# Kernel tuning notes

Hardware: AMD Instinct MI355X
Metric: run time of the kernel (lower is better)

Reference implementation:

```python
import jax, jax.numpy as jnp
import numpy as np

B, N, OBS, H, A = 1024, 64, 128, 256, 16
NH = 4
HD = H // NH


def _linear_params(key, fan_in, fan_out):
    k1, k2 = jax.random.split(key)
    bound = 1.0 / np.sqrt(fan_in)
    W = jax.random.uniform(k1, (fan_out, fan_in), jnp.float32, -bound, bound)
    b = jax.random.uniform(k2, (fan_out,), jnp.float32, -bound, bound)
    return W, b


def setup_inputs() -> dict:
    key = jax.random.key(0)
    ks = jax.random.split(key, 10)
    obs = jax.random.normal(ks[0], (B, N, OBS), jnp.float32)
    adj = jax.random.randint(ks[1], (B, N, N), 0, 2).astype(jnp.float32)
    # guarantee every row has at least one neighbor (self-loop) so softmax is finite
    adj = jnp.maximum(adj, jnp.eye(N, dtype=jnp.float32)[None])
    W1, b1 = _linear_params(ks[2], OBS, H)
    W2, b2 = _linear_params(ks[3], H, H)
    Wq, bq = _linear_params(ks[4], H, H)
    Wk, bk = _linear_params(ks[5], H, H)
    Wv, bv = _linear_params(ks[6], H, H)
    Wo, bo = _linear_params(ks[7], H, H)
    Wc, bc = _linear_params(ks[8], H, H)
    W3, b3 = _linear_params(ks[9], H, A)
    return dict(obs=obs, adj=adj, W1=W1, b1=b1, W2=W2, b2=b2,
                Wq=Wq, bq=bq, Wk=Wk, bk=bk, Wv=Wv, bv=bv,
                Wo=Wo, bo=bo, Wc=Wc, bc=bc, W3=W3, b3=b3)


def reference(obs, adj, W1, b1, W2, b2, Wq, bq, Wk, bk, Wv, bv, Wo, bo, Wc, bc, W3, b3):
    lin = lambda x, W, b: jnp.einsum('bnd,od->bno', x, W) + b
    x = jax.nn.relu(lin(obs, W1, b1))
    x = jax.nn.relu(lin(x, W2, b2))
    # multi-head attention with adjacency mask
    def heads(t):  # [B,N,H] -> [B,NH,N,HD]
        return t.reshape(B, N, NH, HD).transpose(0, 2, 1, 3)
    q = heads(lin(x, Wq, bq))
    k = heads(lin(x, Wk, bk))
    v = heads(lin(x, Wv, bv))
    scores = jnp.einsum('bhqd,bhkd->bhqk', q, k) / np.sqrt(HD).astype(np.float32)
    scores = jnp.where(adj[:, None] == 0, -jnp.inf, scores)
    attn = jax.nn.softmax(scores, axis=-1)
    out = jnp.einsum('bhqk,bhkd->bhqd', attn, v)
    out = out.transpose(0, 2, 1, 3).reshape(B, N, H)
    x = lin(out, Wo, bo)
    # communication: adj @ fc(x)
    x = jnp.einsum('bnm,bmh->bnh', adj, lin(x, Wc, bc))
    return lin(x, W3, b3)
```

## Files before the change

kernel.cpp:

```cpp
#include <hip/hip_runtime.h>
#include <stdint.h>

typedef unsigned short u16;
typedef unsigned long long u64;
typedef __attribute__((ext_vector_type(8))) short short8;
typedef __attribute__((ext_vector_type(4))) float f32x4;

#define MFMA16 __builtin_amdgcn_mfma_f32_16x16x32_bf16

#define MTOT 65536

__device__ __forceinline__ u16 f2bf(float f) {
  union { float f; uint32_t u; } v; v.f = f;
  uint32_t r = v.u + 0x7FFFu + ((v.u >> 16) & 1u);
  return (u16)(r >> 16);
}

union U8 { short8 v; u16 u[8]; };
union U4 { u64 v; u16 u[4]; };

__device__ __forceinline__ void cp16(const void* g, void* l) {
  __builtin_amdgcn_global_load_lds(
      (const __attribute__((address_space(1))) void*)g,
      (__attribute__((address_space(3))) void*)l, 16, 0, 0);
}

__device__ __forceinline__ int swz(int row) { return ((row >> 1) & 3) << 4; }

__global__ __launch_bounds__(256) void k_l1(
    const float* __restrict__ Wc, const float* __restrict__ Wo,
    const float* __restrict__ bo, const float* __restrict__ bc,
    float* __restrict__ M1, float* __restrict__ bv,
    const float* __restrict__ W1, const float* __restrict__ W2,
    const float* __restrict__ Wq, const float* __restrict__ Wk,
    u16* o1, u16* o2, u16* oq, u16* ok,
    const float* __restrict__ adj, u64* __restrict__ adjm_g) {
  const int bid = blockIdx.x, tid = threadIdx.x;
  if (bid < 256) {
    __shared__ float wcr[256];
    __shared__ float red[4];
    const int j = bid, d = tid;
    wcr[d] = Wc[j * 256 + d];
    __syncthreads();
    float acc = 0.f;
    for (int i = 0; i < 256; i++) acc += wcr[i] * Wo[i * 256 + d];
    M1[j * 256 + d] = acc;
    float p = wcr[d] * bo[d];
    for (int off = 32; off >= 1; off >>= 1) p += __shfl_xor(p, off);
    if ((d & 63) == 0) red[d >> 6] = p;
    __syncthreads();
    if (d == 0) bv[j] = bc[j] + red[0] + red[1] + red[2] + red[3];
  } else if (bid < 368) {
    int off8 = (bid - 256) * 256 + tid;
    const float* src; u16* dst;
    if      (off8 <  4096) { src = W1; dst = o1; }
    else if (off8 < 12288) { src = W2; dst = o2; off8 -= 4096; }
    else if (off8 < 20480) { src = Wq; dst = oq; off8 -= 12288; }
    else                   { src = Wk; dst = ok; off8 -= 20480; }
    const int e = off8 * 8;
    f32x4 a = *(const f32x4*)(src + e);
    f32x4 b = *(const f32x4*)(src + e + 4);
    U8 pk;
#pragma unroll
    for (int j = 0; j < 4; j++) { pk.u[j] = f2bf(a[j]); pk.u[4 + j] = f2bf(b[j]); }
    *(short8*)(dst + e) = pk.v;
  } else {
    __shared__ u16 chunk[64][4];
    const int b = bid - 368;
    const int q = tid >> 2, qa = tid & 3;
    const float* ar = adj + ((size_t)b * 64 + q) * 64 + qa * 16;
    f32x4 a0 = *(const f32x4*)(ar);
    f32x4 a1 = *(const f32x4*)(ar + 4);
    f32x4 a2 = *(const f32x4*)(ar + 8);
    f32x4 a3 = *(const f32x4*)(ar + 12);
    unsigned m16 = 0;
#pragma unroll
    for (int i = 0; i < 4; i++) {
      m16 |= (unsigned)(a0[i] != 0.f) << i;
      m16 |= (unsigned)(a1[i] != 0.f) << (4 + i);
      m16 |= (unsigned)(a2[i] != 0.f) << (8 + i);
      m16 |= (unsigned)(a3[i] != 0.f) << (12 + i);
    }
    chunk[q][qa] = (u16)m16;
    __syncthreads();
    if (tid < 64)
      adjm_g[(size_t)b * 64 + tid] =
          (u64)chunk[tid][0] | ((u64)chunk[tid][1] << 16) |
          ((u64)chunk[tid][2] << 32) | ((u64)chunk[tid][3] << 48);
  }
}

template<int K, bool AF32>
__device__ __forceinline__ void gemm_full2(
    const void* __restrict__ Ain, const u16* __restrict__ W,
    const float* __restrict__ bias, u16* __restrict__ C,
    const int m0, const bool relu, char* smem) {
  const int tid = threadIdx.x;
  const int lane = tid & 63, wid = tid >> 6;
  const int wr = wid >> 1, wc = wid & 1;
  const int ro = lane & 15, hi = lane >> 4;

  f32x4 acc0[4][4], acc1[4][4];
#pragma unroll
  for (int m = 0; m < 4; m++)
#pragma unroll
    for (int n = 0; n < 4; n++) {
      acc0[m][n] = (f32x4){0.f, 0.f, 0.f, 0.f};
      acc1[m][n] = (f32x4){0.f, 0.f, 0.f, 0.f};
    }

  auto stage = [&](int buf, int k0) {
    char* Ax = smem + buf * 24576;
    char* Bx = Ax + 8192;
    if (AF32) {
      const float* Af = (const float*)Ain;
#pragma unroll
      for (int it = 0; it < 2; it++) {
        const int e = (tid + it * 256) * 8;
        const int r = e >> 5, c = e & 31;
        const float* s = Af + (size_t)(m0 + r) * K + k0 + c;
        f32x4 a = *(const f32x4*)s, b = *(const f32x4*)(s + 4);
        U8 pk;
#pragma unroll
        for (int j = 0; j < 4; j++) { pk.u[j] = f2bf(a[j]); pk.u[4 + j] = f2bf(b[j]); }
        *(short8*)(Ax + ((r * 64 + c * 2) ^ swz(r))) = pk.v;
      }
    } else {
      const u16* Ab = (const u16*)Ain;
#pragma unroll
      for (int i = 0; i < 2; i++) {
        const int boff = i * 4096 + wid * 1024;
        const int t = boff + lane * 16;
        const int row = t >> 6;
        const int cb = (t & 63) ^ swz(row);
        cp16(Ab + (size_t)(m0 + row) * K + k0 + (cb >> 1), Ax + boff);
      }
    }
#pragma unroll
    for (int i = 0; i < 4; i++) {
      const int boff = i * 4096 + wid * 1024;
      const int t = boff + lane * 16;
      const int row = t >> 6;
      const int cb = (t & 63) ^ swz(row);
      cp16(W + (size_t)row * K + k0 + (cb >> 1), Bx + boff);
    }
  };

  auto compute = [&](int buf) {
    char* Ax = smem + buf * 24576;
    char* Bx = Ax + 8192;
    short8 af[4], fb0[4], fb1[4];
#pragma unroll
    for (int m = 0; m < 4; m++) {
      const int row = wr * 64 + m * 16 + ro;
      af[m] = *(const short8*)(Ax + ((row * 64 + hi * 16) ^ swz(row)));
    }
#pragma unroll
    for (int n = 0; n < 4; n++) {
      const int r0 = wc * 64 + n * 16 + ro;
      fb0[n] = *(const short8*)(Bx + ((r0 * 64 + hi * 16) ^ swz(r0)));
      const int r1 = 128 + r0;
      fb1[n] = *(const short8*)(Bx + ((r1 * 64 + hi * 16) ^ swz(r1)));
    }
    __builtin_amdgcn_s_setprio(1);
#pragma unroll
    for (int m = 0; m < 4; m++)
#pragma unroll
      for (int n = 0; n < 4; n++) {
        acc0[m][n] = MFMA16(af[m], fb0[n], acc0[m][n], 0, 0, 0);
        acc1[m][n] = MFMA16(af[m], fb1[n], acc1[m][n], 0, 0, 0);
      }
    __builtin_amdgcn_s_setprio(0);
  };

  constexpr int NT = K / 32;
  if (AF32) {
    stage(0, 0);
    __syncthreads();
    int cur = 0;
    for (int k0 = 32; k0 < K; k0 += 32) {
      stage(cur ^ 1, k0);
      compute(cur);
      __syncthreads();
      cur ^= 1;
    }
    compute(cur);
    __syncthreads();
  } else {
    stage(0, 0);
    stage(1, 32);
#pragma unroll
    for (int t = 0; t < NT; ++t) {
      if (t == NT - 1) asm volatile("s_waitcnt vmcnt(0)" ::: "memory");
      else             asm volatile("s_waitcnt vmcnt(6)" ::: "memory");
      asm volatile("s_barrier" ::: "memory");
      compute(t & 1);
      asm volatile("s_barrier" ::: "memory");
      if (t + 2 < NT) stage(t & 1, (t + 2) * 32);
    }
  }

  u16 (*Cs)[136] = (u16(*)[136])smem;
  auto ep = [&](f32x4 (&acc)[4][4], const int n0) {
#pragma unroll
    for (int half = 0; half < 2; half++) {
      if (wr == half) {
#pragma unroll
        for (int n = 0; n < 4; n++) {
          const int col = wc * 64 + n * 16 + ro;
          const float bb = bias[n0 + col];
#pragma unroll
          for (int m = 0; m < 4; m++)
#pragma unroll
            for (int j = 0; j < 4; j++) {
              float val = acc[m][n][j] + bb;
              if (relu) val = fmaxf(val, 0.f);
              Cs[m * 16 + hi * 4 + j][col] = f2bf(val);
            }
        }
      }
      __syncthreads();
      for (int i = tid; i < 64 * 16; i += 256) {
        const int r = i >> 4, c = (i & 15) << 3;
        *(short8*)(C + (size_t)(m0 + half * 64 + r) * 256 + n0 + c) = *(short8*)&Cs[r][c];
      }
      __syncthreads();
    }
  };
  ep(acc0, 0);
  ep(acc1, 128);
}

__global__ __launch_bounds__(256, 2) void k_gemm1_prep2(
    const float* __restrict__ obs, const u16* __restrict__ W1b,
    const float* __restrict__ b1, u16* __restrict__ x1,
    const float* __restrict__ W3, const float* __restrict__ M1,
    const float* __restrict__ bvchain, const float* __restrict__ bvw,
    float* __restrict__ Wzf, float* __restrict__ bz) {
  __shared__ char smem[49152];
  if (blockIdx.x < 512) {
    gemm_full2<128, true>(obs, W1b, b1, x1, (int)blockIdx.x * 128, true, smem);
    return;
  }
  float* w3r = (float*)smem;
  float* red = (float*)(smem + 1024);
  const int a = blockIdx.x - 512, d = threadIdx.x;
  w3r[d] = W3[a * 256 + d];
  __syncthreads();
  float acc = 0.f;
  for (int j = 0; j < 256; j++) acc += w3r[j] * M1[j * 256 + d];
  Wzf[a * 256 + d] = acc;
  float p = w3r[d] * bvchain[d] + acc * bvw[d];
  for (int off = 32; off >= 1; off >>= 1) p += __shfl_xor(p, off);
  if ((d & 63) == 0) red[d >> 6] = p;
  __syncthreads();
  if (d == 0) bz[a] = red[0] + red[1] + red[2] + red[3];
}

__global__ __launch_bounds__(256, 2) void k_x2_prep3(
    const u16* __restrict__ x1, const u16* __restrict__ W2b,
    const float* __restrict__ b2, u16* __restrict__ x2,
    const float* __restrict__ Wzf, const float* __restrict__ Wv,
    u16* __restrict__ G) {
  __shared__ char smem[49152];
  if (blockIdx.x < 512) {
    gemm_full2<256, false>(x1, W2b, b2, x2, (int)blockIdx.x * 128, true, smem);
    return;
  }
  const int g = blockIdx.x - 512, d2 = threadIdx.x;
  const int h = g >> 4, a = g & 15;
  float* wzr = (float*)smem;
  if (d2 < 64) wzr[d2] = Wzf[a * 256 + h * 64 + d2];
  __syncthreads();
  float acc = 0.f;
#pragma unroll 8
  for (int d = 0; d < 64; d++) acc += wzr[d] * Wv[(size_t)(h * 64 + d) * 256 + d2];
  G[g * 256 + d2] = f2bf(acc);
}

__global__ __launch_bounds__(256, 2) void k_qk_gemmv(
    const u16* __restrict__ x2,
    const u16* __restrict__ Wqb, const float* __restrict__ bq, u16* __restrict__ Qg,
    const u16* __restrict__ Wkb, const float* __restrict__ bk, u16* __restrict__ Kg,
    const u16* __restrict__ G, u16* __restrict__ Vzt) {
  __shared__ char smem[49152];
  const int bid = blockIdx.x;
  if (bid < 1024) {
    const int q = bid >> 4, r = bid & 15;
    const int mt = q * 8 + (r & 7);
    const int sub = r >> 3;
    gemm_full2<256, false>(x2, sub ? Wkb : Wqb, sub ? bk : bq, sub ? Kg : Qg,
                           mt * 128, false, smem);
    return;
  }
  const int tid = threadIdx.x;
  const int lane = tid & 63, w = tid >> 6;
  const int ro = lane & 15, hi = lane >> 4;
  const int m0 = (bid - 1024) * 128;

  f32x4 acc[2][4];
#pragma unroll
  for (int m = 0; m < 2; m++)
#pragma unroll
    for (int n = 0; n < 4; n++) acc[m][n] = (f32x4){0.f, 0.f, 0.f, 0.f};

  auto stage = [&](int buf, int k0) {
    char* Ax = smem + buf * 12288;
    char* Bx = Ax + 8192;
#pragma unroll
    for (int i = 0; i < 2; i++) {
      const int boff = i * 4096 + w * 1024;
      const int t = boff + lane * 16;
      const int row = t >> 6;
      const int cb = (t & 63) ^ swz(row);
      cp16(x2 + (size_t)(m0 + row) * 256 + k0 + (cb >> 1), Ax + boff);
    }
    {
      const int boff = w * 1024;
      const int t = boff + lane * 16;
      const int row = t >> 6;
      const int cb = (t & 63) ^ swz(row);
      cp16(G + (size_t)row * 256 + k0 + (cb >> 1), Bx + boff);
    }
  };
  auto compute = [&](int buf) {
    char* Ax = smem + buf * 12288;
    char* Bx = Ax + 8192;
    short8 af[2], fb[4];
#pragma unroll
    for (int m = 0; m < 2; m++) {
      const int row = w * 32 + m * 16 + ro;
      af[m] = *(const short8*)(Ax + ((row * 64 + hi * 16) ^ swz(row)));
    }
#pragma unroll
    for (int n = 0; n < 4; n++) {
      const int row = n * 16 + ro;
      fb[n] = *(const short8*)(Bx + ((row * 64 + hi * 16) ^ swz(row)));
    }
    __builtin_amdgcn_s_setprio(1);
#pragma unroll
    for (int m = 0; m < 2; m++)
#pragma unroll
      for (int n = 0; n < 4; n++)
        acc[m][n] = MFMA16(af[m], fb[n], acc[m][n], 0, 0, 0);
    __builtin_amdgcn_s_setprio(0);
  };

  stage(0, 0);
  stage(1, 32);
#pragma unroll
  for (int t = 0; t < 8; ++t) {
    if (t == 7) asm volatile("s_waitcnt vmcnt(0)" ::: "memory");
    else        asm volatile("s_waitcnt vmcnt(3)" ::: "memory");
    asm volatile("s_barrier" ::: "memory");
    compute(t & 1);
    asm volatile("s_barrier" ::: "memory");
    if (t + 2 < 8) stage(t & 1, (t + 2) * 32);
  }

#pragma unroll
  for (int m = 0; m < 2; m++) {
    const int rbase = w * 32 + m * 16;
    const int bidx = (m0 >> 6) + (rbase >> 6);
    const int ke = (rbase + hi * 4) & 63;
#pragma unroll
    for (int n = 0; n < 4; n++) {
      const int c = n * 16 + ro;
      U4 pk;
#pragma unroll
      for (int j = 0; j < 4; j++) pk.u[j] = f2bf(acc[m][n][j]);
      *(u64*)(Vzt + (size_t)bidx * 4096 + (size_t)c * 64 + ke) = pk.v;
    }
  }
}

__global__ __launch_bounds__(256, 2) void attn_fused(
    const u16* __restrict__ Qg, const u16* __restrict__ Kg,
    const u16* __restrict__ Vzt, const u64* __restrict__ adjm_g,
    const float* __restrict__ bz, const float* __restrict__ b3,
    float* __restrict__ out) {
  __shared__ char sm_raw[36864];
  __shared__ u64 adjm[64];
  u16 (*Ps)[64][72] = (u16(*)[64][72])sm_raw;
  float (*Zs)[64][16] = (float(*)[64][16])sm_raw;

  const int b = blockIdx.x, tid = threadIdx.x;
  const int lane = tid & 63, w = tid >> 6;
  const int ro = lane & 15, hi = lane >> 4;
  const int hc = w * 64;
  const size_t base = (size_t)b * 64 * 256;

  if (tid < 64) adjm[tid] = adjm_g[(size_t)b * 64 + tid];

  short8 kb[4][2];
#pragma unroll
  for (int n = 0; n < 4; n++)
#pragma unroll
    for (int ks = 0; ks < 2; ks++)
      kb[n][ks] = *(const short8*)(Kg + base + (size_t)(n * 16 + ro) * 256 + hc + ks * 32 + hi * 8);

  f32x4 s[4][4];
#pragma unroll
  for (int m = 0; m < 4; m++) {
    short8 af[2];
#pragma unroll
    for (int ks = 0; ks < 2; ks++)
      af[ks] = *(const short8*)(Qg + base + (size_t)(m * 16 + ro) * 256 + hc + ks * 32 + hi * 8);
#pragma unroll
    for (int n = 0; n < 4; n++) s[m][n] = (f32x4){0.f, 0.f, 0.f, 0.f};
#pragma unroll
    for (int ks = 0; ks < 2; ks++)
#pragma unroll
      for (int n = 0; n < 4; n++)
        s[m][n] = MFMA16(af[ks], kb[n][ks], s[m][n], 0, 0, 0);
  }

  short8 vz[2];
#pragma unroll
  for (int ks = 0; ks < 2; ks++)
    vz[ks] = *(const short8*)(Vzt + (size_t)b * 4096 + (size_t)(hc / 4 + ro) * 64 + ks * 32 + hi * 8);

  __syncthreads();

#pragma unroll
  for (int m = 0; m < 4; m++) {
#pragma unroll
    for (int j = 0; j < 4; j++) {
      const int q = m * 16 + hi * 4 + j;
      const u64 msk = adjm[q];
      float sv[4], ev[4];
      float mx = -3.0e38f;
#pragma unroll
      for (int n = 0; n < 4; n++) {
        const bool on = (msk >> (n * 16 + ro)) & 1ull;
        sv[n] = on ? s[m][n][j] * 0.125f : -3.0e38f;
        mx = fmaxf(mx, sv[n]);
      }
      mx = fmaxf(mx, __shfl_xor(mx, 1));
      mx = fmaxf(mx, __shfl_xor(mx, 2));
      mx = fmaxf(mx, __shfl_xor(mx, 4));
      mx = fmaxf(mx, __shfl_xor(mx, 8));
      float sum = 0.f;
#pragma unroll
      for (int n = 0; n < 4; n++) {
        ev[n] = (sv[n] > -1.0e37f) ? __expf(sv[n] - mx) : 0.f;
        sum += ev[n];
      }
      sum += __shfl_xor(sum, 1);
      sum += __shfl_xor(sum, 2);
      sum += __shfl_xor(sum, 4);
      sum += __shfl_xor(sum, 8);
      const float inv = 1.0f / sum;
#pragma unroll
      for (int n = 0; n < 4; n++)
        Ps[w][q][n * 16 + ro] = f2bf(ev[n] * inv);
    }
  }

  f32x4 oz[4];
#pragma unroll
  for (int m = 0; m < 4; m++) {
    short8 pa[2];
    pa[0] = *(const short8*)&Ps[w][m * 16 + ro][hi * 8];
    pa[1] = *(const short8*)&Ps[w][m * 16 + ro][32 + hi * 8];
    oz[m] = (f32x4){0.f, 0.f, 0.f, 0.f};
#pragma unroll
    for (int ks = 0; ks < 2; ks++)
      oz[m] = MFMA16(pa[ks], vz[ks], oz[m], 0, 0, 0);
  }
  __syncthreads();

#pragma unroll
  for (int m = 0; m < 4; m++)
#pragma unroll
    for (int j = 0; j < 4; j++)
      Zs[w][m * 16 + hi * 4 + j][ro] = oz[m][j];
  __syncthreads();

  for (int i = tid; i < 1024; i += 256) {
    const int r = i >> 4, a = i & 15;
    Zs[0][r][a] += Zs[1][r][a] + Zs[2][r][a] + Zs[3][r][a];
  }
  __syncthreads();

  {
    const int n = tid >> 2, a4 = (tid & 3) << 2;
    const u64 msk = adjm[n];
    const float deg = (float)__popcll(msk);
    float a0 = 0.f, a1 = 0.f, a2 = 0.f, a3 = 0.f;
#pragma unroll 8
    for (int m = 0; m < 64; m++) {
      const float wv = (float)((msk >> m) & 1ull);
      f32x4 z = *(const f32x4*)&Zs[0][m][a4];
      a0 += wv * z[0]; a1 += wv * z[1]; a2 += wv * z[2]; a3 += wv * z[3];
    }
    f32x4 r;
    r[0] = a0 + b3[a4 + 0] + deg * bz[a4 + 0];
    r[1] = a1 + b3[a4 + 1] + deg * bz[a4 + 1];
    r[2] = a2 + b3[a4 + 2] + deg * bz[a4 + 2];
    r[3] = a3 + b3[a4 + 3] + deg * bz[a4 + 3];
    *(f32x4*)(out + ((size_t)b * 64 + n) * 16 + a4) = r;
  }
}

extern "C" void kernel_launch(void* const* d_in, const int* in_sizes, int n_in,
                              void* d_out, int out_size, void* d_ws, size_t ws_size,
                              hipStream_t stream) {
  const float* obs = (const float*)d_in[0];
  const float* adj = (const float*)d_in[1];
  const float* W1  = (const float*)d_in[2];
  const float* b1  = (const float*)d_in[3];
  const float* W2  = (const float*)d_in[4];
  const float* b2  = (const float*)d_in[5];
  const float* Wq  = (const float*)d_in[6];
  const float* bq  = (const float*)d_in[7];
  const float* Wk  = (const float*)d_in[8];
  const float* bk  = (const float*)d_in[9];
  const float* Wv  = (const float*)d_in[10];
  const float* bvw = (const float*)d_in[11];
  const float* Wo  = (const float*)d_in[12];
  const float* bo  = (const float*)d_in[13];
  const float* Wc  = (const float*)d_in[14];
  const float* bc  = (const float*)d_in[15];
  const float* W3  = (const float*)d_in[16];
  const float* b3  = (const float*)d_in[17];
  float* out = (float*)d_out;

  char* ws = (char*)d_ws;
  const size_t BIG = (size_t)MTOT * 256 * 2;
  u16* buf0 = (u16*)(ws);
  u16* buf1 = (u16*)(ws + BIG);
  u16* buf2 = (u16*)(ws + 2 * BIG);
  u16* buf3 = (u16*)(ws + 3 * BIG);
  char* p = ws + 4 * BIG;
  u16* W1b = (u16*)p;              p += 128 * 256 * 2;
  u16* W2b = (u16*)p;              p += 256 * 256 * 2;
  u16* Wqb = (u16*)p;              p += 256 * 256 * 2;
  u16* Wkb = (u16*)p;              p += 256 * 256 * 2;
  float* M1 = (float*)p;           p += 256 * 256 * 4;
  float* Wzf = (float*)p;          p += 16 * 256 * 4;
  u16* G   = (u16*)p;              p += 64 * 256 * 2;
  float* bv = (float*)p;           p += 256 * 4;
  float* bz = (float*)p;           p += 16 * 4;
  u64* adjm_g = (u64*)p;           p += (size_t)MTOT * 8;

  dim3 blk(256);
  k_l1<<<dim3(1392), blk, 0, stream>>>(Wc, Wo, bo, bc, M1, bv,
                                       W1, W2, Wq, Wk, W1b, W2b, Wqb, Wkb,
                                       adj, adjm_g);
  k_gemm1_prep2<<<dim3(528), blk, 0, stream>>>(obs, W1b, b1, buf0,
                                               W3, M1, bv, bvw, Wzf, bz);
  k_x2_prep3<<<dim3(576), blk, 0, stream>>>(buf0, W2b, b2, buf1, Wzf, Wv, G);
  k_qk_gemmv<<<dim3(1536), blk, 0, stream>>>(buf1, Wqb, bq, buf2,
                                             Wkb, bk, buf3, G, buf0);
  attn_fused<<<dim3(1024), blk, 0, stream>>>(buf2, buf3, buf0, adjm_g, bz, b3, out);
}
```

Before: 118.9 us.

## Fuse Vz projection into x2 GEMM epilogue and fold G prep into layer1 kernel

The x2 GEMM epilogue now stages bf16 output tiles in LDS and immediately multiplies them by the G matrix with MFMA to produce Vzt. This removes the separate GEMV blocks that re-read x2 from global memory in the QK kernel. The G computation moves into the prep blocks of the first GEMM kernel, which drops the intermediate Wzf buffer and one launch's worth of small blocks. In exchange, the epilogue of the x2 GEMM does extra LDS loads and MFMA work, and Vzt gets its own workspace buffer instead of reusing buf0.

```diff
diff --git a/kernel.cpp b/kernel.cpp
--- a/kernel.cpp
+++ b/kernel.cpp
@@ -90,11 +90,12 @@
   }
 }
 
-template<int K, bool AF32>
+template<int K, bool AF32, bool VZ>
 __device__ __forceinline__ void gemm_full2(
     const void* __restrict__ Ain, const u16* __restrict__ W,
     const float* __restrict__ bias, u16* __restrict__ C,
-    const int m0, const bool relu, char* smem) {
+    const int m0, const bool relu, char* smem,
+    const u16* __restrict__ Gw, u16* __restrict__ Vzt) {
   const int tid = threadIdx.x;
   const int lane = tid & 63, wid = tid >> 6;
   const int wr = wid >> 1, wc = wid & 1;
@@ -108,6 +109,13 @@
       acc0[m][n] = (f32x4){0.f, 0.f, 0.f, 0.f};
       acc1[m][n] = (f32x4){0.f, 0.f, 0.f, 0.f};
     }
+  f32x4 vzacc[2][4];
+  if (VZ) {
+#pragma unroll
+    for (int h = 0; h < 2; h++)
+#pragma unroll
+      for (int cf = 0; cf < 4; cf++) vzacc[h][cf] = (f32x4){0.f, 0.f, 0.f, 0.f};
+  }
 
   auto stage = [&](int buf, int k0) {
     char* Ax = smem + buf * 24576;
@@ -201,7 +209,18 @@
   }
 
   u16 (*Cs)[136] = (u16(*)[136])smem;
+  char* Gl = smem + 18432;
   auto ep = [&](f32x4 (&acc)[4][4], const int n0) {
+    if (VZ) {
+#pragma unroll
+      for (int i = 0; i < 4; i++) {
+        const int boff = i * 4096 + wid * 1024;
+        const int t = boff + lane * 16;
+        const int row = t >> 8;
+        const int cb = (t & 255) ^ ((row & 7) << 4);
+        cp16(Gw + (size_t)row * 256 + n0 + (cb >> 1), Gl + boff);
+      }
+    }
 #pragma unroll
     for (int half = 0; half < 2; half++) {
       if (wr == half) {
@@ -224,11 +243,39 @@
         const int r = i >> 4, c = (i & 15) << 3;
         *(short8*)(C + (size_t)(m0 + half * 64 + r) * 256 + n0 + c) = *(short8*)&Cs[r][c];
       }
+      if (VZ) {
+#pragma unroll
+        for (int ks = 0; ks < 4; ks++) {
+          short8 af = *(const short8*)&Cs[wid * 16 + ro][ks * 32 + hi * 8];
+#pragma unroll
+          for (int cf = 0; cf < 4; cf++) {
+            const int c = cf * 16 + ro;
+            short8 gb = *(const short8*)(Gl + ((c * 256 + (ks * 32 + hi * 8) * 2) ^ ((c & 7) << 4)));
+            vzacc[half][cf] = MFMA16(af, gb, vzacc[half][cf], 0, 0, 0);
+          }
+        }
+      }
       __syncthreads();
     }
   };
   ep(acc0, 0);
   ep(acc1, 128);
+
+  if (VZ) {
+#pragma unroll
+    for (int half = 0; half < 2; half++) {
+      const int bidx = (m0 >> 6) + half;
+      const int ke = wid * 16 + hi * 4;
+#pragma unroll
+      for (int cf = 0; cf < 4; cf++) {
+        const int c = cf * 16 + ro;
+        U4 pk;
+#pragma unroll
+        for (int j = 0; j < 4; j++) pk.u[j] = f2bf(vzacc[half][cf][j]);
+        *(u64*)(Vzt + (size_t)bidx * 4096 + (size_t)c * 64 + ke) = pk.v;
+      }
+    }
+  }
 }
 
 __global__ __launch_bounds__(256, 2) void k_gemm1_prep2(
@@ -236,142 +283,59 @@
     const float* __restrict__ b1, u16* __restrict__ x1,
     const float* __restrict__ W3, const float* __restrict__ M1,
     const float* __restrict__ bvchain, const float* __restrict__ bvw,
-    float* __restrict__ Wzf, float* __restrict__ bz) {
+    const float* __restrict__ Wv, u16* __restrict__ G,
+    float* __restrict__ bz) {
   __shared__ char smem[49152];
   if (blockIdx.x < 512) {
-    gemm_full2<128, true>(obs, W1b, b1, x1, (int)blockIdx.x * 128, true, smem);
+    gemm_full2<128, true, false>(obs, W1b, b1, x1, (int)blockIdx.x * 128,
+                                 true, smem, nullptr, nullptr);
     return;
   }
   float* w3r = (float*)smem;
-  float* red = (float*)(smem + 1024);
+  float* wzs = (float*)(smem + 1024);
+  float* red = (float*)(smem + 2048);
   const int a = blockIdx.x - 512, d = threadIdx.x;
   w3r[d] = W3[a * 256 + d];
   __syncthreads();
   float acc = 0.f;
   for (int j = 0; j < 256; j++) acc += w3r[j] * M1[j * 256 + d];
-  Wzf[a * 256 + d] = acc;
+  wzs[d] = acc;
   float p = w3r[d] * bvchain[d] + acc * bvw[d];
   for (int off = 32; off >= 1; off >>= 1) p += __shfl_xor(p, off);
   if ((d & 63) == 0) red[d >> 6] = p;
   __syncthreads();
   if (d == 0) bz[a] = red[0] + red[1] + red[2] + red[3];
-}
-
-__global__ __launch_bounds__(256, 2) void k_x2_prep3(
+#pragma unroll
+  for (int h = 0; h < 4; h++) {
+    float g = 0.f;
+#pragma unroll 8
+    for (int d2 = 0; d2 < 64; d2++)
+      g += wzs[h * 64 + d2] * Wv[(size_t)(h * 64 + d2) * 256 + d];
+    G[(size_t)(h * 16 + a) * 256 + d] = f2bf(g);
+  }
+}
+
+__global__ __launch_bounds__(256, 2) void k_x2_vz(
     const u16* __restrict__ x1, const u16* __restrict__ W2b,
     const float* __restrict__ b2, u16* __restrict__ x2,
-    const float* __restrict__ Wzf, const float* __restrict__ Wv,
-    u16* __restrict__ G) {
+    const u16* __restrict__ G, u16* __restrict__ Vzt) {
   __shared__ char smem[49152];
-  if (blockIdx.x < 512) {
-    gemm_full2<256, false>(x1, W2b, b2, x2, (int)blockIdx.x * 128, true, smem);
-    return;
-  }
-  const int g = blockIdx.x - 512, d2 = threadIdx.x;
-  const int h = g >> 4, a = g & 15;
-  float* wzr = (float*)smem;
-  if (d2 < 64) wzr[d2] = Wzf[a * 256 + h * 64 + d2];
-  __syncthreads();
-  float acc = 0.f;
-#pragma unroll 8
-  for (int d = 0; d < 64; d++) acc += wzr[d] * Wv[(size_t)(h * 64 + d) * 256 + d2];
-  G[g * 256 + d2] = f2bf(acc);
-}
-
-__global__ __launch_bounds__(256, 2) void k_qk_gemmv(
+  gemm_full2<256, false, true>(x1, W2b, b2, x2, (int)blockIdx.x * 128,
+                               true, smem, G, Vzt);
+}
+
+__global__ __launch_bounds__(256, 2) void k_qk(
     const u16* __restrict__ x2,
     const u16* __restrict__ Wqb, const float* __restrict__ bq, u16* __restrict__ Qg,
-    const u16* __restrict__ Wkb, const float* __restrict__ bk, u16* __restrict__ Kg,
-    const u16* __restrict__ G, u16* __restrict__ Vzt) {
+    const u16* __restrict__ Wkb, const float* __restrict__ bk, u16* __restrict__ Kg) {
   __shared__ char smem[49152];
   const int bid = blockIdx.x;
-  if (bid < 1024) {
-    const int q = bid >> 4, r = bid & 15;
-    const int mt = q * 8 + (r & 7);
-    const int sub = r >> 3;
-    gemm_full2<256, false>(x2, sub ? Wkb : Wqb, sub ? bk : bq, sub ? Kg : Qg,
-                           mt * 128, false, smem);
-    return;
-  }
-  const int tid = threadIdx.x;
-  const int lane = tid & 63, w = tid >> 6;
-  const int ro = lane & 15, hi = lane >> 4;
-  const int m0 = (bid - 1024) * 128;
-
-  f32x4 acc[2][4];
-#pragma unroll
-  for (int m = 0; m < 2; m++)
-#pragma unroll
-    for (int n = 0; n < 4; n++) acc[m][n] = (f32x4){0.f, 0.f, 0.f, 0.f};
-
-  auto stage = [&](int buf, int k0) {
-    char* Ax = smem + buf * 12288;
-    char* Bx = Ax + 8192;
-#pragma unroll
-    for (int i = 0; i < 2; i++) {
-      const int boff = i * 4096 + w * 1024;
-      const int t = boff + lane * 16;
-      const int row = t >> 6;
-      const int cb = (t & 63) ^ swz(row);
-      cp16(x2 + (size_t)(m0 + row) * 256 + k0 + (cb >> 1), Ax + boff);
-    }
-    {
-      const int boff = w * 1024;
-      const int t = boff + lane * 16;
-      const int row = t >> 6;
-      const int cb = (t & 63) ^ swz(row);
-      cp16(G + (size_t)row * 256 + k0 + (cb >> 1), Bx + boff);
-    }
-  };
-  auto compute = [&](int buf) {
-    char* Ax = smem + buf * 12288;
-    char* Bx = Ax + 8192;
-    short8 af[2], fb[4];
-#pragma unroll
-    for (int m = 0; m < 2; m++) {
-      const int row = w * 32 + m * 16 + ro;
-      af[m] = *(const short8*)(Ax + ((row * 64 + hi * 16) ^ swz(row)));
-    }
-#pragma unroll
-    for (int n = 0; n < 4; n++) {
-      const int row = n * 16 + ro;
-      fb[n] = *(const short8*)(Bx + ((row * 64 + hi * 16) ^ swz(row)));
-    }
-    __builtin_amdgcn_s_setprio(1);
-#pragma unroll
-    for (int m = 0; m < 2; m++)
-#pragma unroll
-      for (int n = 0; n < 4; n++)
-        acc[m][n] = MFMA16(af[m], fb[n], acc[m][n], 0, 0, 0);
-    __builtin_amdgcn_s_setprio(0);
-  };
-
-  stage(0, 0);
-  stage(1, 32);
-#pragma unroll
-  for (int t = 0; t < 8; ++t) {
-    if (t == 7) asm volatile("s_waitcnt vmcnt(0)" ::: "memory");
-    else        asm volatile("s_waitcnt vmcnt(3)" ::: "memory");
-    asm volatile("s_barrier" ::: "memory");
-    compute(t & 1);
-    asm volatile("s_barrier" ::: "memory");
-    if (t + 2 < 8) stage(t & 1, (t + 2) * 32);
-  }
-
-#pragma unroll
-  for (int m = 0; m < 2; m++) {
-    const int rbase = w * 32 + m * 16;
-    const int bidx = (m0 >> 6) + (rbase >> 6);
-    const int ke = (rbase + hi * 4) & 63;
-#pragma unroll
-    for (int n = 0; n < 4; n++) {
-      const int c = n * 16 + ro;
-      U4 pk;
-#pragma unroll
-      for (int j = 0; j < 4; j++) pk.u[j] = f2bf(acc[m][n][j]);
-      *(u64*)(Vzt + (size_t)bidx * 4096 + (size_t)c * 64 + ke) = pk.v;
-    }
-  }
+  const int q = bid >> 4, r = bid & 15;
+  const int mt = q * 8 + (r & 7);
+  const int sub = r >> 3;
+  gemm_full2<256, false, false>(x2, sub ? Wkb : Wqb, sub ? bk : bq,
+                                sub ? Kg : Qg, mt * 128, false, smem,
+                                nullptr, nullptr);
 }
 
 __global__ __launch_bounds__(256, 2) void attn_fused(
@@ -538,20 +502,19 @@
   u16* Wqb = (u16*)p;              p += 256 * 256 * 2;
   u16* Wkb = (u16*)p;              p += 256 * 256 * 2;
   float* M1 = (float*)p;           p += 256 * 256 * 4;
-  float* Wzf = (float*)p;          p += 16 * 256 * 4;
   u16* G   = (u16*)p;              p += 64 * 256 * 2;
   float* bv = (float*)p;           p += 256 * 4;
   float* bz = (float*)p;           p += 16 * 4;
   u64* adjm_g = (u64*)p;           p += (size_t)MTOT * 8;
+  u16* Vzt = (u16*)p;              p += (size_t)MTOT * 64 * 2;
 
   dim3 blk(256);
   k_l1<<<dim3(1392), blk, 0, stream>>>(Wc, Wo, bo, bc, M1, bv,
                                        W1, W2, Wq, Wk, W1b, W2b, Wqb, Wkb,
                                        adj, adjm_g);
   k_gemm1_prep2<<<dim3(528), blk, 0, stream>>>(obs, W1b, b1, buf0,
-                                               W3, M1, bv, bvw, Wzf, bz);
-  k_x2_prep3<<<dim3(576), blk, 0, stream>>>(buf0, W2b, b2, buf1, Wzf, Wv, G);
-  k_qk_gemmv<<<dim3(1536), blk, 0, stream>>>(buf1, Wqb, bq, buf2,
-                                             Wkb, bk, buf3, G, buf0);
-  attn_fused<<<dim3(1024), blk, 0, stream>>>(buf2, buf3, buf0, adjm_g, bz, b3, out);
-}
+                                               W3, M1, bv, bvw, Wv, G, bz);
+  k_x2_vz<<<dim3(512), blk, 0, stream>>>(buf0, W2b, b2, buf1, G, Vzt);
+  k_qk<<<dim3(1024), blk, 0, stream>>>(buf1, Wqb, bq, buf2, Wkb, bk, buf3);
+  attn_fused<<<dim3(1024), blk, 0, stream>>>(buf2, buf3, Vzt, adjm_g, bz, b3, out);
+}
```

After: 123.0 us. 1.03x slower.
